# Kernel tuning notes

Hardware: AMD Instinct MI355X
Metric: run time of the kernel (lower is better)

The kernel has to match this reference:

```python
import jax, jax.numpy as jnp
import numpy as np

EPS_FP32 = 1e-8
MASK_VALUE = -1.0e9
D_MODEL = 1024
N_HEADS = 16
D_K = D_MODEL // N_HEADS
SCALE = 1.0 / np.sqrt(D_K)


def stable_softmax(x, axis=-1):
    x_max = jnp.max(x, axis=axis, keepdims=True)
    e = jnp.exp(x - x_max)
    return e / (jnp.sum(e, axis=axis, keepdims=True) + EPS_FP32)


def setup_inputs() -> dict:
    key = jax.random.key(0)
    ks = jax.random.split(key, 10)
    B, S, D = 2, 2048, D_MODEL
    x = jax.random.normal(ks[0], (B, S, D), dtype=jnp.float32)
    # causal mask, broadcastable to [B, H, S, S]; 0 -> masked
    mask = jnp.tril(jnp.ones((S, S), dtype=jnp.int32))[None, None, :, :]
    w_scale = 0.02
    Wq = jax.random.normal(ks[1], (D, D), dtype=jnp.float32) * w_scale
    Wk = jax.random.normal(ks[2], (D, D), dtype=jnp.float32) * w_scale
    Wv = jax.random.normal(ks[3], (D, D), dtype=jnp.float32) * w_scale
    Wo = jax.random.normal(ks[4], (D, D), dtype=jnp.float32) * (w_scale * 0.2)
    bq = jnp.zeros((D,), dtype=jnp.float32)
    bk = jnp.zeros((D,), dtype=jnp.float32)
    bv = jnp.zeros((D,), dtype=jnp.float32)
    bo = jnp.zeros((D,), dtype=jnp.float32)
    return {"x": x, "Wq": Wq, "bq": bq, "Wk": Wk, "bk": bk,
            "Wv": Wv, "bv": bv, "Wo": Wo, "bo": bo, "mask": mask}


def reference(x, Wq, bq, Wk, bk, Wv, bv, Wo, bo, mask):
    B, S, D = x.shape
    H, Dk = N_HEADS, D_K
    # torch nn.Linear: y = x @ W.T + b
    def proj(W, b):
        y = jnp.einsum('bsd,ed->bse', x, W) + b
        return y.reshape(B, S, H, Dk).transpose(0, 2, 1, 3)  # [B,H,S,Dk]
    Q = proj(Wq, bq)
    K = proj(Wk, bk)
    V = proj(Wv, bv)
    scores = jnp.einsum('bhqd,bhkd->bhqk', Q, K) * SCALE  # [B,H,S,S]
    scores = jnp.where(mask == 0, MASK_VALUE, scores)
    attn = stable_softmax(scores, axis=-1)
    out = jnp.einsum('bhqk,bhkd->bhqd', attn, V)  # [B,H,S,Dk]
    out = out.transpose(0, 2, 1, 3).reshape(B, S, D)
    return jnp.einsum('bsd,ed->bse', out, Wo) + bo
```

## Files before the change

kernel.cpp:

```cpp
#include <hip/hip_runtime.h>
#include <math.h>

typedef float v4f __attribute__((ext_vector_type(4)));
typedef __bf16 v8y __attribute__((ext_vector_type(8)));
typedef __attribute__((address_space(1))) const void av1_t;
typedef __attribute__((address_space(3))) void av3_t;
typedef unsigned short u16;

#define SCALE_ 0.125f
#define MASKV_ (-1.0e9f)

__device__ __forceinline__ u16 bfhi(float f) {
  union { float f; unsigned u; } v; v.f = f;
  return (u16)(v.u >> 16);
}
__device__ __forceinline__ float bf2f(u16 h) {
  union { unsigned u; float f; } v; v.u = ((unsigned)h) << 16;
  return v.f;
}
__device__ __forceinline__ v4f mfma16(v8y a, v8y b, v4f c) {
  return __builtin_amdgcn_mfma_f32_16x16x32_bf16(a, b, c, 0, 0, 0);
}
__device__ __forceinline__ void gload16(const void* g, void* l) {
  __builtin_amdgcn_global_load_lds((av1_t*)g, (av3_t*)l, 16, 0, 0);
}

__global__ __launch_bounds__(256) void split_kernel(const float* __restrict__ src,
                                                    u16* __restrict__ dst) {
  const int idx = blockIdx.x * 256 + threadIdx.x;
  const int row = idx >> 8, c4 = idx & 255;
  const float4 v = ((const float4*)src)[idx];
  const u16 h0 = bfhi(v.x), h1 = bfhi(v.y), h2 = bfhi(v.z), h3 = bfhi(v.w);
  ushort4 hi, lo;
  hi.x = h0; hi.y = h1; hi.z = h2; hi.w = h3;
  lo.x = bfhi(v.x - bf2f(h0)); lo.y = bfhi(v.y - bf2f(h1));
  lo.z = bfhi(v.z - bf2f(h2)); lo.w = bfhi(v.w - bf2f(h3));
  *(ushort4*)&dst[(size_t)row * 2048 + c4 * 4] = hi;
  *(ushort4*)&dst[(size_t)row * 2048 + 1024 + c4 * 4] = lo;
}

__global__ __launch_bounds__(256) void gemm_kernel(
    const u16* __restrict__ A2, const u16* __restrict__ B2,
    const float* __restrict__ bias0, const float* __restrict__ bias1,
    const float* __restrict__ bias2,
    float* __restrict__ outF,
    u16* __restrict__ Q2, u16* __restrict__ K2,
    u16* __restrict__ Vthi, u16* __restrict__ Vtlo,
    int ntiles_n, int mode)
{
  __shared__ __align__(16) u16 sm[16384];
  const int tid = threadIdx.x;
  const int lane = tid & 63;
  const int wid = tid >> 6;
  const int wm = wid >> 1, wn = wid & 1;

  int bid = blockIdx.x;
  const int cpx = gridDim.x >> 3;
  bid = (bid & 7) * cpx + (bid >> 3);
  const int mt = bid / ntiles_n, nt = bid % ntiles_n;
  const int m0 = mt * 128, n0 = nt * 128;

  v4f acc[4][4];
  #pragma unroll
  for (int i = 0; i < 4; ++i)
    #pragma unroll
    for (int j = 0; j < 4; ++j) { v4f z = {0.f, 0.f, 0.f, 0.f}; acc[i][j] = z; }

  for (int t = 0; t < 48; ++t) {
    const int aoff = (t < 16 ? t : t - 16) * 64;
    const int boff = (t < 32 ? t : t - 32) * 64;
    __syncthreads();
    #pragma unroll
    for (int p = 0; p < 4; ++p) {
      const int u = p * 256 + tid;
      const int row = u >> 3, cph = u & 7;
      const int clog = cph ^ (row & 7);
      char* lbaseA = (char*)sm + (p * 256 + wid * 64) * 16;
      char* lbaseB = (char*)sm + 16384 + (p * 256 + wid * 64) * 16;
      gload16(&A2[(size_t)(m0 + row) * 2048 + aoff + clog * 8], lbaseA);
      gload16(&B2[(size_t)(n0 + row) * 2048 + boff + clog * 8], lbaseB);
    }
    __syncthreads();
    #pragma unroll
    for (int kc = 0; kc < 2; ++kc) {
      v8y af[4];
      #pragma unroll
      for (int i = 0; i < 4; ++i) {
        const int row = wm * 64 + i * 16 + (lane & 15);
        const int ch = (kc * 4 + (lane >> 4)) ^ (row & 7);
        af[i] = *(const v8y*)((const char*)sm + row * 128 + ch * 16);
      }
      #pragma unroll
      for (int j = 0; j < 4; ++j) {
        const int row = wn * 64 + j * 16 + (lane & 15);
        const int ch = (kc * 4 + (lane >> 4)) ^ (row & 7);
        const v8y bf = *(const v8y*)((const char*)sm + 16384 + row * 128 + ch * 16);
        #pragma unroll
        for (int i = 0; i < 4; ++i)
          acc[i][j] = mfma16(af[i], bf, acc[i][j]);
      }
    }
  }

  #pragma unroll
  for (int i = 0; i < 4; ++i) {
    #pragma unroll
    for (int j = 0; j < 4; ++j) {
      #pragma unroll
      for (int r = 0; r < 4; ++r) {
        const int m = m0 + wm * 64 + i * 16 + (lane >> 4) * 4 + r;
        const int n = n0 + wn * 64 + j * 16 + (lane & 15);
        float y = acc[i][j][r];
        if (mode == 0) {
          outF[(size_t)m * 1024 + n] = y + bias0[n];
        } else {
          const int which = n >> 10;
          const int nn = n & 1023;
          const int hh = nn >> 6, dk = n & 63;
          const int b = m >> 11, s = m & 2047;
          y += (which == 0 ? bias0[nn] : (which == 1 ? bias1[nn] : bias2[nn]));
          const u16 hi = bfhi(y);
          const u16 lo = bfhi(y - bf2f(hi));
          const size_t bh = (size_t)(b * 16 + hh);
          if (which == 2) {
            const size_t a = (bh * 64 + dk) * 2048 + s;
            Vthi[a] = hi; Vtlo[a] = lo;
          } else {
            u16* dst = (which == 0) ? Q2 : K2;
            const size_t a = (bh * 2048 + s) * 128 + dk;
            dst[a] = hi; dst[a + 64] = lo;
          }
        }
      }
    }
  }
}

__global__ __launch_bounds__(256) void attn_kernel(
    const u16* __restrict__ Q2, const u16* __restrict__ K2,
    const u16* __restrict__ Vthi, const u16* __restrict__ Vtlo,
    u16* __restrict__ ctx2)
{
  __shared__ __align__(16) u16 sm[24576];
  const int tid = threadIdx.x, lane = tid & 63, wid = tid >> 6;
  const int h = blockIdx.y, b = blockIdx.z;
  const size_t bh = (size_t)(b * 16 + h);
  const u16* Qb = Q2 + bh * 2048 * 128;
  const u16* Kb = K2 + bh * 2048 * 128;
  const u16* Vhb = Vthi + bh * (size_t)64 * 2048;
  const u16* Vlb = Vtlo + bh * (size_t)64 * 2048;

  #pragma unroll 1
  for (int half = 0; half < 2; ++half) {
    const int qt = (half == 0) ? (int)blockIdx.x : 31 - (int)blockIdx.x;
    const int q0 = qt * 64;

    v8y qf[4];
    #pragma unroll
    for (int pc = 0; pc < 4; ++pc)
      qf[pc] = *(const v8y*)&Qb[(size_t)(q0 + wid * 16 + (lane & 15)) * 128
                                + pc * 32 + (lane >> 4) * 8];

    v4f o[4];
    float mrun[4], lrun[4];
    #pragma unroll
    for (int nb = 0; nb < 4; ++nb) { v4f z = {0.f,0.f,0.f,0.f}; o[nb] = z; }
    #pragma unroll
    for (int r = 0; r < 4; ++r) { mrun[r] = -INFINITY; lrun[r] = 0.f; }

    for (int kb = 0; kb <= qt; ++kb) {
      const int k0 = kb * 64;
      __syncthreads();
      #pragma unroll
      for (int p = 0; p < 4; ++p) {
        const int u = p * 256 + tid;
        const int row = u >> 4, c = u & 15;
        const int cph = c ^ (row & 7);
        const uint4 kv = *(const uint4*)&Kb[(size_t)(k0 + row) * 128 + c * 8];
        *(uint4*)((char*)sm + row * 256 + cph * 16) = kv;
        const uint4 vv = (c < 8)
            ? *(const uint4*)&Vhb[(size_t)row * 2048 + k0 + c * 8]
            : *(const uint4*)&Vlb[(size_t)row * 2048 + k0 + (c - 8) * 8];
        *(uint4*)((char*)sm + 16384 + row * 256 + cph * 16) = vv;
      }
      __syncthreads();

      v4f s[4];
      #pragma unroll
      for (int nb = 0; nb < 4; ++nb) { v4f z = {0.f,0.f,0.f,0.f}; s[nb] = z; }
      #pragma unroll
      for (int kc = 0; kc < 6; ++kc) {
        const int ma = (kc < 2) ? kc : kc - 2;
        const int mb = (kc < 4) ? kc : kc - 4;
        #pragma unroll
        for (int nb = 0; nb < 4; ++nb) {
          const int row = nb * 16 + (lane & 15);
          const int ch = (mb * 4 + (lane >> 4)) ^ (row & 7);
          const v8y kf = *(const v8y*)((const char*)sm + row * 256 + ch * 16);
          s[nb] = mfma16(qf[ma], kf, s[nb]);
        }
      }

      const bool domask = (kb == qt);
      float alpha[4];
      char* pbase = (char*)sm + 32768 + wid * 4096;
      #pragma unroll
      for (int r = 0; r < 4; ++r) {
        float sv[4];
        #pragma unroll
        for (int nb = 0; nb < 4; ++nb) {
          float v = s[nb][r] * SCALE_;
          if (domask) {
            const int qg = q0 + wid * 16 + (lane >> 4) * 4 + r;
            const int kg = k0 + nb * 16 + (lane & 15);
            if (kg > qg) v = MASKV_;
          }
          sv[nb] = v;
        }
        float rm = fmaxf(fmaxf(sv[0], sv[1]), fmaxf(sv[2], sv[3]));
        rm = fmaxf(rm, __shfl_xor(rm, 1));
        rm = fmaxf(rm, __shfl_xor(rm, 2));
        rm = fmaxf(rm, __shfl_xor(rm, 4));
        rm = fmaxf(rm, __shfl_xor(rm, 8));
        const float mnew = fmaxf(mrun[r], rm);
        const float al = __expf(mrun[r] - mnew);
        const int pr = (lane >> 4) * 4 + r;
        char* prow = pbase + pr * 256;
        float ls = 0.f;
        #pragma unroll
        for (int nb = 0; nb < 4; ++nb) {
          const float pv = __expf(sv[nb] - mnew);
          ls += pv;
          const u16 phi = bfhi(pv);
          const u16 plo = bfhi(pv - bf2f(phi));
          const int kp = nb * 16 + (lane & 15);
          *(u16*)(prow + (((kp >> 3)       ^ (pr & 7)) * 16) + (kp & 7) * 2) = phi;
          *(u16*)(prow + (((8 + (kp >> 3)) ^ (pr & 7)) * 16) + (kp & 7) * 2) = plo;
        }
        ls += __shfl_xor(ls, 1);
        ls += __shfl_xor(ls, 2);
        ls += __shfl_xor(ls, 4);
        ls += __shfl_xor(ls, 8);
        lrun[r] = lrun[r] * al + ls;
        mrun[r] = mnew;
        alpha[r] = al;
      }
      #pragma unroll
      for (int nb = 0; nb < 4; ++nb)
        #pragma unroll
        for (int r = 0; r < 4; ++r)
          o[nb][r] *= alpha[r];

      #pragma unroll
      for (int kc = 0; kc < 6; ++kc) {
        const int ma = (kc < 2) ? kc : kc - 2;
        const int mb = (kc < 4) ? kc : kc - 4;
        const int prow_r = lane & 15;
        const int pch = (ma * 4 + (lane >> 4)) ^ (prow_r & 7);
        const v8y pf = *(const v8y*)(pbase + prow_r * 256 + pch * 16);
        #pragma unroll
        for (int nb = 0; nb < 4; ++nb) {
          const int row = nb * 16 + (lane & 15);
          const int ch = (mb * 4 + (lane >> 4)) ^ (row & 7);
          const v8y vf = *(const v8y*)((const char*)sm + 16384 + row * 256 + ch * 16);
          o[nb] = mfma16(pf, vf, o[nb]);
        }
      }
    }

    #pragma unroll
    for (int r = 0; r < 4; ++r) {
      const float inv = 1.0f / (lrun[r] + 1e-8f);
      const int q = q0 + wid * 16 + (lane >> 4) * 4 + r;
      const size_t mrow = (size_t)(b * 2048 + q) * 2048;
      #pragma unroll
      for (int nb = 0; nb < 4; ++nb) {
        const float y = o[nb][r] * inv;
        const u16 hi = bfhi(y);
        const u16 lo = bfhi(y - bf2f(hi));
        const int col = h * 64 + nb * 16 + (lane & 15);
        ctx2[mrow + col] = hi;
        ctx2[mrow + 1024 + col] = lo;
      }
    }
  }
}

extern "C" void kernel_launch(void* const* d_in, const int* in_sizes, int n_in,
                              void* d_out, int out_size, void* d_ws, size_t ws_size,
                              hipStream_t stream)
{
  const float* x  = (const float*)d_in[0];
  const float* Wq = (const float*)d_in[1];
  const float* bq = (const float*)d_in[2];
  const float* Wk = (const float*)d_in[3];
  const float* bk = (const float*)d_in[4];
  const float* Wv = (const float*)d_in[5];
  const float* bv = (const float*)d_in[6];
  const float* Wo = (const float*)d_in[7];
  const float* bo = (const float*)d_in[8];

  u16* wsp  = (u16*)d_ws;
  u16* Q2   = wsp;
  u16* K2   = Q2 + (size_t)32 * 2048 * 128;
  u16* Vthi = K2 + (size_t)32 * 2048 * 128;
  u16* Vtlo = Vthi + (size_t)32 * 64 * 2048;
  u16* ctx2 = Vtlo + (size_t)32 * 64 * 2048;
  u16* W2   = ctx2;
  u16* Wo2  = Q2;
  u16* X2   = (u16*)d_out;

  split_kernel<<<4096, 256, 0, stream>>>(x, X2);
  split_kernel<<<1024, 256, 0, stream>>>(Wq, W2);
  split_kernel<<<1024, 256, 0, stream>>>(Wk, W2 + (size_t)1024 * 2048);
  split_kernel<<<1024, 256, 0, stream>>>(Wv, W2 + (size_t)2048 * 2048);

  gemm_kernel<<<768, 256, 0, stream>>>(X2, W2, bq, bk, bv,
                                       nullptr, Q2, K2, Vthi, Vtlo, 24, 1);

  attn_kernel<<<dim3(16, 16, 2), 256, 0, stream>>>(Q2, K2, Vthi, Vtlo, ctx2);

  split_kernel<<<1024, 256, 0, stream>>>(Wo, Wo2);

  gemm_kernel<<<256, 256, 0, stream>>>(ctx2, Wo2, bo, nullptr, nullptr,
                                       (float*)d_out, nullptr, nullptr, nullptr, nullptr,
                                       8, 0);
}
```

Baseline: 434.7 us.

## Add 256x256 eight-wave pipelined GEMM for fused QKV projection

Replaces the 128x128 four-wave GEMM used for the QKV projection with a new 256x256 tile kernel of 512 threads. It double-buffers K-chunks in 128 KB of LDS through direct global-to-LDS loads, interleaves prefetch with MFMA phases, and raises wave priority around the MFMA blocks. The K-loop covers the hi/lo split (hi*hi, hi*lo, lo*hi passes) in 48 steps. The larger tile cuts global traffic per FLOP and hides load latency, but it launches only 192 blocks, which may leave CUs underused, and it carries heavy register pressure.

```diff
diff --git a/kernel.cpp b/kernel.cpp
--- a/kernel.cpp
+++ b/kernel.cpp
@@ -39,14 +39,179 @@
   *(ushort4*)&dst[(size_t)row * 2048 + 1024 + c4 * 4] = lo;
 }
 
-__global__ __launch_bounds__(256) void gemm_kernel(
+__global__ __launch_bounds__(512, 2) void gemm8_kernel(
     const u16* __restrict__ A2, const u16* __restrict__ B2,
     const float* __restrict__ bias0, const float* __restrict__ bias1,
     const float* __restrict__ bias2,
-    float* __restrict__ outF,
     u16* __restrict__ Q2, u16* __restrict__ K2,
-    u16* __restrict__ Vthi, u16* __restrict__ Vtlo,
-    int ntiles_n, int mode)
+    u16* __restrict__ Vthi, u16* __restrict__ Vtlo)
+{
+  __shared__ __align__(16) u16 sm[65536];
+  char* smc = (char*)sm;
+  const int tid = threadIdx.x, lane = tid & 63, wid = tid >> 6;
+  const int wm = wid >> 2, wn = wid & 3;
+  const int l15 = lane & 15, ck = lane >> 4;
+
+  int bid = blockIdx.x;
+  const int cpx = gridDim.x >> 3;
+  bid = (bid & 7) * cpx + (bid >> 3);
+  const int mt = bid / 12, nt = bid % 12;
+  const int m0 = mt * 256, n0 = nt * 256;
+
+  int offA[8], offB[4];
+  #pragma unroll
+  for (int i = 0; i < 8; ++i) {
+    const int row = wm * 128 + i * 16 + l15;
+    offA[i] = row * 64 + (((ck + ((row >> 1) & 3)) & 3) * 16);
+  }
+  #pragma unroll
+  for (int j = 0; j < 4; ++j) {
+    const int row = wn * 64 + j * 16 + l15;
+    offB[j] = row * 64 + (((ck + ((row >> 1) & 3)) & 3) * 16);
+  }
+
+  const int srow = tid >> 2, spc = tid & 3;
+  const int sc = (spc - ((srow >> 1) & 3)) & 3;
+  const size_t gA0 = (size_t)(m0 + srow) * 2048 + sc * 8;
+  const size_t gB0 = (size_t)(n0 + srow) * 2048 + sc * 8;
+  const int ldst0 = wid * 64 * 16;
+
+  #define STAGE_(G, gbase, col, lds_off)                                      \
+    do {                                                                      \
+      gload16(&G[(gbase) + (col)], smc + (lds_off) + ldst0);                  \
+      gload16(&G[(gbase) + (col) + 128 * 2048], smc + (lds_off) + ldst0 + 8192); \
+    } while (0)
+
+  v4f acc[8][4];
+  #pragma unroll
+  for (int i = 0; i < 8; ++i)
+    #pragma unroll
+    for (int j = 0; j < 4; ++j) { v4f z = {0.f, 0.f, 0.f, 0.f}; acc[i][j] = z; }
+
+  {
+    const int a0 = 0, b0 = 0;
+    STAGE_(A2, gA0, a0, 0);
+    STAGE_(B2, gB0, b0, 65536);
+    STAGE_(A2, gA0, a0 + 32, 16384);
+    STAGE_(B2, gB0, b0 + 32, 65536 + 16384);
+  }
+  asm volatile("s_waitcnt vmcnt(4)" ::: "memory");
+  __builtin_amdgcn_s_barrier();
+
+  #pragma unroll 1
+  for (int t = 0; t < 48; ++t) {
+    const int buf = t & 1;
+    const char* Ac0 = smc + buf * 32768;
+    const char* Bc0 = smc + 65536 + buf * 32768;
+    const char* Ac1 = Ac0 + 16384;
+    const char* Bc1 = Bc0 + 16384;
+    const int nbA = (buf ^ 1) * 32768;
+    const int nbB = 65536 + (buf ^ 1) * 32768;
+    const int t1 = t + 1;
+    const bool pf = (t1 < 48);
+    const int an = (t1 < 32 ? 0 : 1024) + (t1 & 15) * 64;
+    const int bn = ((t1 >= 16 && t1 < 32) ? 1024 : 0) + (t1 & 15) * 64;
+
+    v8y a[4], b[4];
+    #pragma unroll
+    for (int i = 0; i < 4; ++i) a[i] = *(const v8y*)(Ac0 + offA[i]);
+    #pragma unroll
+    for (int j = 0; j < 4; ++j) b[j] = *(const v8y*)(Bc0 + offB[j]);
+    if (pf) STAGE_(A2, gA0, an, nbA);
+    __builtin_amdgcn_s_barrier();
+    __builtin_amdgcn_s_setprio(1);
+    #pragma unroll
+    for (int j = 0; j < 4; ++j)
+      #pragma unroll
+      for (int i = 0; i < 4; ++i)
+        acc[i][j] = mfma16(a[i], b[j], acc[i][j]);
+    __builtin_amdgcn_s_setprio(0);
+    __builtin_amdgcn_s_barrier();
+
+    #pragma unroll
+    for (int i = 0; i < 4; ++i) a[i] = *(const v8y*)(Ac0 + offA[4 + i]);
+    if (pf) {
+      STAGE_(B2, gB0, bn, nbB);
+      asm volatile("s_waitcnt vmcnt(4)" ::: "memory");
+    } else {
+      asm volatile("s_waitcnt vmcnt(0)" ::: "memory");
+    }
+    __builtin_amdgcn_s_barrier();
+    __builtin_amdgcn_s_setprio(1);
+    #pragma unroll
+    for (int j = 0; j < 4; ++j)
+      #pragma unroll
+      for (int i = 0; i < 4; ++i)
+        acc[4 + i][j] = mfma16(a[i], b[j], acc[4 + i][j]);
+    __builtin_amdgcn_s_setprio(0);
+    __builtin_amdgcn_s_barrier();
+
+    #pragma unroll
+    for (int i = 0; i < 4; ++i) a[i] = *(const v8y*)(Ac1 + offA[i]);
+    #pragma unroll
+    for (int j = 0; j < 4; ++j) b[j] = *(const v8y*)(Bc1 + offB[j]);
+    if (pf) STAGE_(A2, gA0, an + 32, nbA + 16384);
+    __builtin_amdgcn_s_barrier();
+    __builtin_amdgcn_s_setprio(1);
+    #pragma unroll
+    for (int j = 0; j < 4; ++j)
+      #pragma unroll
+      for (int i = 0; i < 4; ++i)
+        acc[i][j] = mfma16(a[i], b[j], acc[i][j]);
+    __builtin_amdgcn_s_setprio(0);
+    __builtin_amdgcn_s_barrier();
+
+    #pragma unroll
+    for (int i = 0; i < 4; ++i) a[i] = *(const v8y*)(Ac1 + offA[4 + i]);
+    if (pf) {
+      STAGE_(B2, gB0, bn + 32, nbB + 16384);
+      asm volatile("s_waitcnt vmcnt(4)" ::: "memory");
+    }
+    __builtin_amdgcn_s_barrier();
+    __builtin_amdgcn_s_setprio(1);
+    #pragma unroll
+    for (int j = 0; j < 4; ++j)
+      #pragma unroll
+      for (int i = 0; i < 4; ++i)
+        acc[4 + i][j] = mfma16(a[i], b[j], acc[4 + i][j]);
+    __builtin_amdgcn_s_setprio(0);
+    __builtin_amdgcn_s_barrier();
+  }
+  #undef STAGE_
+
+  #pragma unroll
+  for (int i = 0; i < 8; ++i) {
+    #pragma unroll
+    for (int j = 0; j < 4; ++j) {
+      #pragma unroll
+      for (int r = 0; r < 4; ++r) {
+        const int m = m0 + wm * 128 + i * 16 + (lane >> 4) * 4 + r;
+        const int n = n0 + wn * 64 + j * 16 + l15;
+        float y = acc[i][j][r];
+        const int which = n >> 10, nn = n & 1023;
+        const int hh = nn >> 6, dk = n & 63;
+        const int b_ = m >> 11, s = m & 2047;
+        y += (which == 0 ? bias0[nn] : (which == 1 ? bias1[nn] : bias2[nn]));
+        const u16 hi = bfhi(y);
+        const u16 lo = bfhi(y - bf2f(hi));
+        const size_t bh = (size_t)(b_ * 16 + hh);
+        if (which == 2) {
+          const size_t a_ = (bh * 64 + dk) * 2048 + s;
+          Vthi[a_] = hi; Vtlo[a_] = lo;
+        } else {
+          u16* dst = (which == 0) ? Q2 : K2;
+          const size_t a_ = (bh * 2048 + s) * 128 + dk;
+          dst[a_] = hi; dst[a_ + 64] = lo;
+        }
+      }
+    }
+  }
+}
+
+__global__ __launch_bounds__(256) void gemm_kernel(
+    const u16* __restrict__ A2, const u16* __restrict__ B2,
+    const float* __restrict__ bias0,
+    float* __restrict__ outF, int ntiles_n)
 {
   __shared__ __align__(16) u16 sm[16384];
   const int tid = threadIdx.x;
@@ -110,27 +275,7 @@
       for (int r = 0; r < 4; ++r) {
         const int m = m0 + wm * 64 + i * 16 + (lane >> 4) * 4 + r;
         const int n = n0 + wn * 64 + j * 16 + (lane & 15);
-        float y = acc[i][j][r];
-        if (mode == 0) {
-          outF[(size_t)m * 1024 + n] = y + bias0[n];
-        } else {
-          const int which = n >> 10;
-          const int nn = n & 1023;
-          const int hh = nn >> 6, dk = n & 63;
-          const int b = m >> 11, s = m & 2047;
-          y += (which == 0 ? bias0[nn] : (which == 1 ? bias1[nn] : bias2[nn]));
-          const u16 hi = bfhi(y);
-          const u16 lo = bfhi(y - bf2f(hi));
-          const size_t bh = (size_t)(b * 16 + hh);
-          if (which == 2) {
-            const size_t a = (bh * 64 + dk) * 2048 + s;
-            Vthi[a] = hi; Vtlo[a] = lo;
-          } else {
-            u16* dst = (which == 0) ? Q2 : K2;
-            const size_t a = (bh * 2048 + s) * 128 + dk;
-            dst[a] = hi; dst[a + 64] = lo;
-          }
-        }
+        outF[(size_t)m * 1024 + n] = acc[i][j][r] + bias0[n];
       }
     }
   }
@@ -315,14 +460,12 @@
   split_kernel<<<1024, 256, 0, stream>>>(Wk, W2 + (size_t)1024 * 2048);
   split_kernel<<<1024, 256, 0, stream>>>(Wv, W2 + (size_t)2048 * 2048);
 
-  gemm_kernel<<<768, 256, 0, stream>>>(X2, W2, bq, bk, bv,
-                                       nullptr, Q2, K2, Vthi, Vtlo, 24, 1);
+  gemm8_kernel<<<192, 512, 0, stream>>>(X2, W2, bq, bk, bv,
+                                        Q2, K2, Vthi, Vtlo);
 
   attn_kernel<<<dim3(16, 16, 2), 256, 0, stream>>>(Q2, K2, Vthi, Vtlo, ctx2);
 
   split_kernel<<<1024, 256, 0, stream>>>(Wo, Wo2);
 
-  gemm_kernel<<<256, 256, 0, stream>>>(ctx2, Wo2, bo, nullptr, nullptr,
-                                       (float*)d_out, nullptr, nullptr, nullptr, nullptr,
-                                       8, 0);
-}
+  gemm_kernel<<<256, 256, 0, stream>>>(ctx2, Wo2, bo, (float*)d_out, 8);
+}
```

Result: faster. 412.4 us (-5.1%).

## Restructure split-bf16 GEMM to load hi/lo tiles together and reuse fragments

Applied to the files above, without the earlier changes.

The three-term bf16x3 GEMM previously streamed 48 separate K-tiles (A_hi·B_hi, A_lo·B_hi, A_hi·B_lo), reloading A and B each time. It now loads the A hi/lo and B hi/lo 32-wide slices into LDS together in 32 steps and reuses the B-hi and A-hi fragments across two of the three products, using a new 4-chunk swizzle with precomputed offsets. The three weight-split launches are also merged into one kernel. This cuts global-to-LDS traffic and barrier count per MFMA, at the cost of a narrower K step per iteration and a new swizzle pattern.

```diff
diff --git a/kernel.cpp b/kernel.cpp
--- a/kernel.cpp
+++ b/kernel.cpp
@@ -39,7 +39,25 @@
   *(ushort4*)&dst[(size_t)row * 2048 + 1024 + c4 * 4] = lo;
 }
 
-__global__ __launch_bounds__(256) void gemm_kernel(
+__global__ __launch_bounds__(256) void splitw_kernel(
+    const float* __restrict__ Wq, const float* __restrict__ Wk,
+    const float* __restrict__ Wv, u16* __restrict__ dst) {
+  const int r = blockIdx.x;
+  const int c4 = threadIdx.x;
+  const float* src = (r < 1024) ? Wq + (size_t)r * 1024
+                   : (r < 2048) ? Wk + (size_t)(r - 1024) * 1024
+                                : Wv + (size_t)(r - 2048) * 1024;
+  const float4 v = ((const float4*)src)[c4];
+  const u16 h0 = bfhi(v.x), h1 = bfhi(v.y), h2 = bfhi(v.z), h3 = bfhi(v.w);
+  ushort4 hi, lo;
+  hi.x = h0; hi.y = h1; hi.z = h2; hi.w = h3;
+  lo.x = bfhi(v.x - bf2f(h0)); lo.y = bfhi(v.y - bf2f(h1));
+  lo.z = bfhi(v.z - bf2f(h2)); lo.w = bfhi(v.w - bf2f(h3));
+  *(ushort4*)&dst[(size_t)r * 2048 + c4 * 4] = hi;
+  *(ushort4*)&dst[(size_t)r * 2048 + 1024 + c4 * 4] = lo;
+}
+
+__global__ __launch_bounds__(256) void gemm3_kernel(
     const u16* __restrict__ A2, const u16* __restrict__ B2,
     const float* __restrict__ bias0, const float* __restrict__ bias1,
     const float* __restrict__ bias2,
@@ -49,10 +67,12 @@
     int ntiles_n, int mode)
 {
   __shared__ __align__(16) u16 sm[16384];
+  char* smc = (char*)sm;
   const int tid = threadIdx.x;
   const int lane = tid & 63;
   const int wid = tid >> 6;
   const int wm = wid >> 1, wn = wid & 1;
+  const int l15 = lane & 15, ck = lane >> 4;
 
   int bid = blockIdx.x;
   const int cpx = gridDim.x >> 3;
@@ -60,46 +80,71 @@
   const int mt = bid / ntiles_n, nt = bid % ntiles_n;
   const int m0 = mt * 128, n0 = nt * 128;
 
+  int offA[4], offB[4];
+  #pragma unroll
+  for (int i = 0; i < 4; ++i) {
+    const int row = wm * 64 + i * 16 + l15;
+    offA[i] = row * 64 + (((ck + ((row >> 1) & 3)) & 3) * 16);
+  }
+  #pragma unroll
+  for (int j = 0; j < 4; ++j) {
+    const int row = wn * 64 + j * 16 + l15;
+    offB[j] = row * 64 + (((ck + ((row >> 1) & 3)) & 3) * 16);
+  }
+
   v4f acc[4][4];
   #pragma unroll
   for (int i = 0; i < 4; ++i)
     #pragma unroll
     for (int j = 0; j < 4; ++j) { v4f z = {0.f, 0.f, 0.f, 0.f}; acc[i][j] = z; }
 
-  for (int t = 0; t < 48; ++t) {
-    const int aoff = (t < 16 ? t : t - 16) * 64;
-    const int boff = (t < 32 ? t : t - 32) * 64;
+  #pragma unroll 1
+  for (int s = 0; s < 32; ++s) {
     __syncthreads();
     #pragma unroll
-    for (int p = 0; p < 4; ++p) {
-      const int u = p * 256 + tid;
-      const int row = u >> 3, cph = u & 7;
-      const int clog = cph ^ (row & 7);
-      char* lbaseA = (char*)sm + (p * 256 + wid * 64) * 16;
-      char* lbaseB = (char*)sm + 16384 + (p * 256 + wid * 64) * 16;
-      gload16(&A2[(size_t)(m0 + row) * 2048 + aoff + clog * 8], lbaseA);
-      gload16(&B2[(size_t)(n0 + row) * 2048 + boff + clog * 8], lbaseB);
+    for (int p = 0; p < 8; ++p) {
+      const int w = (p & 1) * 256 + tid;
+      const int row = w >> 2, cph = w & 3;
+      const int clog = (cph - ((row >> 1) & 3)) & 3;
+      const int qi = p >> 1;
+      const u16* src = (qi < 2) ? A2 : B2;
+      const int r0 = (qi < 2) ? m0 : n0;
+      const int qoff = (qi & 1) * 1024;
+      gload16(&src[(size_t)(r0 + row) * 2048 + qoff + s * 32 + clog * 8],
+              smc + p * 4096 + wid * 1024);
     }
     __syncthreads();
-    #pragma unroll
-    for (int kc = 0; kc < 2; ++kc) {
-      v8y af[4];
-      #pragma unroll
-      for (int i = 0; i < 4; ++i) {
-        const int row = wm * 64 + i * 16 + (lane & 15);
-        const int ch = (kc * 4 + (lane >> 4)) ^ (row & 7);
-        af[i] = *(const v8y*)((const char*)sm + row * 128 + ch * 16);
-      }
-      #pragma unroll
-      for (int j = 0; j < 4; ++j) {
-        const int row = wn * 64 + j * 16 + (lane & 15);
-        const int ch = (kc * 4 + (lane >> 4)) ^ (row & 7);
-        const v8y bf = *(const v8y*)((const char*)sm + 16384 + row * 128 + ch * 16);
-        #pragma unroll
-        for (int i = 0; i < 4; ++i)
-          acc[i][j] = mfma16(af[i], bf, acc[i][j]);
-      }
-    }
+
+    v8y bhi[4], af[4];
+    #pragma unroll
+    for (int j = 0; j < 4; ++j) bhi[j] = *(const v8y*)(smc + 16384 + offB[j]);
+
+    #pragma unroll
+    for (int i = 0; i < 4; ++i) af[i] = *(const v8y*)(smc + offA[i]);
+    #pragma unroll
+    for (int j = 0; j < 4; ++j)
+      #pragma unroll
+      for (int i = 0; i < 4; ++i)
+        acc[i][j] = mfma16(af[i], bhi[j], acc[i][j]);
+
+    #pragma unroll
+    for (int i = 0; i < 4; ++i) af[i] = *(const v8y*)(smc + 8192 + offA[i]);
+    #pragma unroll
+    for (int j = 0; j < 4; ++j)
+      #pragma unroll
+      for (int i = 0; i < 4; ++i)
+        acc[i][j] = mfma16(af[i], bhi[j], acc[i][j]);
+
+    v8y blo[4];
+    #pragma unroll
+    for (int j = 0; j < 4; ++j) blo[j] = *(const v8y*)(smc + 24576 + offB[j]);
+    #pragma unroll
+    for (int i = 0; i < 4; ++i) af[i] = *(const v8y*)(smc + offA[i]);
+    #pragma unroll
+    for (int j = 0; j < 4; ++j)
+      #pragma unroll
+      for (int i = 0; i < 4; ++i)
+        acc[i][j] = mfma16(af[i], blo[j], acc[i][j]);
   }
 
   #pragma unroll
@@ -117,17 +162,17 @@
           const int which = n >> 10;
           const int nn = n & 1023;
           const int hh = nn >> 6, dk = n & 63;
-          const int b = m >> 11, s = m & 2047;
+          const int b = m >> 11, sr = m & 2047;
           y += (which == 0 ? bias0[nn] : (which == 1 ? bias1[nn] : bias2[nn]));
           const u16 hi = bfhi(y);
           const u16 lo = bfhi(y - bf2f(hi));
           const size_t bh = (size_t)(b * 16 + hh);
           if (which == 2) {
-            const size_t a = (bh * 64 + dk) * 2048 + s;
+            const size_t a = (bh * 64 + dk) * 2048 + sr;
             Vthi[a] = hi; Vtlo[a] = lo;
           } else {
             u16* dst = (which == 0) ? Q2 : K2;
-            const size_t a = (bh * 2048 + s) * 128 + dk;
+            const size_t a = (bh * 2048 + sr) * 128 + dk;
             dst[a] = hi; dst[a + 64] = lo;
           }
         }
@@ -311,18 +356,16 @@
   u16* X2   = (u16*)d_out;
 
   split_kernel<<<4096, 256, 0, stream>>>(x, X2);
-  split_kernel<<<1024, 256, 0, stream>>>(Wq, W2);
-  split_kernel<<<1024, 256, 0, stream>>>(Wk, W2 + (size_t)1024 * 2048);
-  split_kernel<<<1024, 256, 0, stream>>>(Wv, W2 + (size_t)2048 * 2048);
-
-  gemm_kernel<<<768, 256, 0, stream>>>(X2, W2, bq, bk, bv,
-                                       nullptr, Q2, K2, Vthi, Vtlo, 24, 1);
+  splitw_kernel<<<3072, 256, 0, stream>>>(Wq, Wk, Wv, W2);
+
+  gemm3_kernel<<<768, 256, 0, stream>>>(X2, W2, bq, bk, bv,
+                                        nullptr, Q2, K2, Vthi, Vtlo, 24, 1);
 
   attn_kernel<<<dim3(16, 16, 2), 256, 0, stream>>>(Q2, K2, Vthi, Vtlo, ctx2);
 
   split_kernel<<<1024, 256, 0, stream>>>(Wo, Wo2);
 
-  gemm_kernel<<<256, 256, 0, stream>>>(ctx2, Wo2, bo, nullptr, nullptr,
-                                       (float*)d_out, nullptr, nullptr, nullptr, nullptr,
-                                       8, 0);
-}
+  gemm3_kernel<<<256, 256, 0, stream>>>(ctx2, Wo2, bo, nullptr, nullptr,
+                                        (float*)d_out, nullptr, nullptr, nullptr, nullptr,
+                                        8, 0);
+}
```

Result: faster. 391.9 us (-9.8%).
